# Performance work log

Measured on AMD Instinct MI355X. Metric: run time of the kernel, lower is better.

Reference implementation:

```python
import jax, jax.numpy as jnp
import numpy as np

D, FIN1, CL1_F, CL1_K, CL2_F, CL2_K, FC1_F, FC2_F = 4096, 1, 32, 25, 64, 25, 512, 10
B = 64
NNZ1, NNZ2 = D * 8, (D // 2) * 8
LMAX = 2.0  # lmax_L of a normalized graph Laplacian
FC1FIN = CL2_F * (D // 4)


def setup_inputs() -> dict:
    key = jax.random.key(0)
    ks = jax.random.split(key, 16)
    def lin(kw, fout, fin):
        scale = np.sqrt(2.0 / (fin + fout)).astype(np.float32)
        return jax.random.uniform(kw, (fout, fin), jnp.float32, -scale, scale)
    V2 = D // 2
    return {
        "x": jax.random.normal(ks[0], (B, D, FIN1), jnp.float32),
        "L1_rows": jax.random.randint(ks[1], (NNZ1,), 0, D),
        "L1_cols": jax.random.randint(ks[2], (NNZ1,), 0, D),
        "L1_vals": jax.random.normal(ks[3], (NNZ1,), jnp.float32) * 0.1,
        "L2_rows": jax.random.randint(ks[4], (NNZ2,), 0, V2),
        "L2_cols": jax.random.randint(ks[5], (NNZ2,), 0, V2),
        "L2_vals": jax.random.normal(ks[6], (NNZ2,), jnp.float32) * 0.1,
        "cl1_W": lin(ks[7], CL1_F, CL1_K * FIN1),
        "cl1_b": jnp.zeros((CL1_F,), jnp.float32),
        "cl2_W": lin(ks[8], CL2_F, CL2_K * CL1_F),
        "cl2_b": jnp.zeros((CL2_F,), jnp.float32),
        "fc1_W": lin(ks[9], FC1_F, FC1FIN),
        "fc1_b": jnp.zeros((FC1_F,), jnp.float32),
        "fc2_W": lin(ks[10], FC2_F, FC1_F),
        "fc2_b": jnp.zeros((FC2_F,), jnp.float32),
    }


def _cheby_conv(x, rows, cols, vals, W, b, K):
    # x: [B, V, Fin]; sparse rescaled Laplacian Ls = (2/lmax)*L - I applied as SpMM.
    Bn, V, Fin = x.shape
    x0 = jnp.transpose(x, (1, 2, 0)).reshape(V, Fin * Bn)  # [V, Fin*B]
    coef = jnp.asarray(2.0 / LMAX, x.dtype)

    def Ls(z):  # (2/lmax) * L @ z - z, via segment-sum SpMM
        return coef * jax.ops.segment_sum(vals[:, None] * z[cols], rows, num_segments=V) - z

    xs = [x0]
    if K > 1:
        x1 = Ls(x0)
        xs.append(x1)
    for _ in range(2, K):
        x2 = 2.0 * Ls(x1) - x0
        xs.append(x2)
        x0, x1 = x1, x2
    xk = jnp.stack(xs, 0).reshape(K, V, Fin, Bn)        # [K, V, Fin, B]
    xk = jnp.transpose(xk, (3, 1, 2, 0)).reshape(Bn * V, Fin * K)
    y = xk @ W.T + b
    return y.reshape(Bn, V, -1)


def _max_pool(x, p):
    # max-pool over node dim with stride p (matches MaxPool1d over permuted layout)
    Bn, V, F = x.shape
    return x.reshape(Bn, V // p, p, F).max(axis=2)


def reference(x, L1_rows, L1_cols, L1_vals, L2_rows, L2_cols, L2_vals,
              cl1_W, cl1_b, cl2_W, cl2_b, fc1_W, fc1_b, fc2_W, fc2_b):
    h = _cheby_conv(x, L1_rows, L1_cols, L1_vals, cl1_W, cl1_b, CL1_K)
    h = jax.nn.relu(h)
    h = _max_pool(h, 2)
    h = _cheby_conv(h, L2_rows, L2_cols, L2_vals, cl2_W, cl2_b, CL2_K)
    h = jax.nn.relu(h)
    h = _max_pool(h, 2)
    h = h.reshape(-1, FC1FIN)
    h = jax.nn.relu(h @ fc1_W.T + fc1_b)
    # dropout d=0.0 (eval/deterministic) -> identity
    return h @ fc2_W.T + fc2_b
```

## Files before the change

kernel.cpp:

```cpp
#include <hip/hip_runtime.h>
#include <hip/hip_bf16.h>

#define V1 4096
#define V2 2048
#define NNZ1 32768
#define NNZ2 16384
#define WCAP 48

typedef unsigned short u16;
typedef unsigned int u32;
typedef __attribute__((ext_vector_type(8))) short bf16x8;
typedef __attribute__((ext_vector_type(4))) float f32x4;

static __device__ __forceinline__ float bf2f(u16 u) {
  union { u32 i; float f; } c; c.i = ((u32)u) << 16; return c.f;
}
static __device__ __forceinline__ u16 f2bf(float f) {
  union { u32 i; float f; } c; c.f = f;
  u32 r = c.i + 0x7FFFu + ((c.i >> 16) & 1u);
  return (u16)(r >> 16);
}

__global__ void k_hist(const int* __restrict__ L1r, const int* __restrict__ L2r,
                       const float* __restrict__ W2, u16* __restrict__ Wh,
                       u16* __restrict__ Wl,
                       int* __restrict__ cnt1, int* __restrict__ cnt2) {
  int lt = blockIdx.x, t = threadIdx.x;
  if (lt < 128) {
    atomicAdd(&cnt1[L1r[lt * 256 + t]], 1);
  } else if (lt < 192) {
    atomicAdd(&cnt2[L2r[(lt - 128) * 256 + t]], 1);
  } else {
    int idx = (lt - 192) * 256 + t;
    int f = idx / 800;
    int kap = idx - f * 800;
    int k = kap >> 5, fin = kap & 31;
    float w = W2[f * 800 + fin * 25 + k];
    u16 hi = f2bf(w);
    Wh[idx] = hi;
    Wl[idx] = f2bf(w - bf2f(hi));
  }
}

__global__ void k_scan(int* __restrict__ cnt1, int* __restrict__ rs1,
                       int* __restrict__ cnt2, int* __restrict__ rs2,
                       int* __restrict__ slotOf1, int* __restrict__ rowOf1,
                       int* __restrict__ slotOf2, int* __restrict__ rowOf2) {
  __shared__ int sums[256];
  __shared__ int degS[V1];
  __shared__ int hist[64];
  __shared__ int hb[64];
  int t = threadIdx.x;
  int* cnt; int* rs; int* slotOf; int* rowOf; int V, NT, nnz;
  if (blockIdx.x == 0) { cnt = cnt1; rs = rs1; slotOf = slotOf1; rowOf = rowOf1; V = V1; NT = 1024; nnz = NNZ1; }
  else                 { cnt = cnt2; rs = rs2; slotOf = slotOf2; rowOf = rowOf2; V = V2; NT = 512;  nnz = NNZ2; }
  int chunk = V / 256, base = t * chunk, s = 0;
  for (int i = 0; i < chunk; ++i) { int c = cnt[base + i]; degS[base + i] = c; s += c; }
  sums[t] = s;
  if (t < 64) hist[t] = 0;
  __syncthreads();
  if (t == 0) {
    int run = 0;
    for (int i = 0; i < 256; ++i) { int c = sums[i]; sums[i] = run; run += c; }
  }
  __syncthreads();
  int pfx = sums[t];
  for (int i = 0; i < chunk; ++i) {
    int c = degS[base + i];
    rs[base + i] = pfx;
    cnt[base + i] = pfx;
    pfx += c;
  }
  if (t == 0) rs[V] = nnz;
  for (int i = 0; i < chunk; ++i) {
    int d = degS[base + i]; if (d > 63) d = 63;
    atomicAdd(&hist[d], 1);
  }
  __syncthreads();
  if (t == 0) {
    int run = 0;
    for (int d = 63; d >= 0; --d) { hb[d] = run; run += hist[d]; }
  }
  __syncthreads();
  for (int i = 0; i < chunk; ++i) {
    int v = base + i;
    int d = degS[v]; if (d > 63) d = 63;
    int r = atomicAdd(&hb[d], 1);
    int slot = (r & 3) * NT + (r >> 2);
    slotOf[v] = slot;
    rowOf[slot] = v;
  }
}

__global__ void k_scatter(const int* __restrict__ L1r, const int* __restrict__ L1c,
                          const float* __restrict__ L1v,
                          const int* __restrict__ L2r, const int* __restrict__ L2c,
                          const float* __restrict__ L2v,
                          int* __restrict__ cur1, const int* __restrict__ rs1,
                          const int* __restrict__ slotOf1, float2* __restrict__ ell1,
                          int* __restrict__ cur2, const int* __restrict__ rs2,
                          const int* __restrict__ slotOf2, float2* __restrict__ ell2) {
  int lt = blockIdx.x, t = threadIdx.x;
  if (lt < 128) {
    int e = lt * 256 + t;
    int row = L1r[e];
    int pos = atomicAdd(&cur1[row], 1);
    int w = pos - rs1[row];
    if (w < WCAP)
      ell1[(size_t)w * V1 + slotOf1[row]] = make_float2(L1v[e], __int_as_float(L1c[e] * 4));
  } else {
    int e = (lt - 128) * 256 + t;
    int row = L2r[e];
    int pos = atomicAdd(&cur2[row], 1);
    int w = pos - rs2[row];
    if (w < WCAP)
      ell2[(size_t)w * V2 + slotOf2[row]] = make_float2(L2v[e], __int_as_float(L2c[e] * 16));
  }
}

__global__ void __launch_bounds__(1024) k_l1rec(
    const float* __restrict__ x, const int* __restrict__ rs1,
    const int* __restrict__ rowOf1, const float2* __restrict__ ell1,
    u16* __restrict__ T1) {
  __shared__ float fa[V1];
  const int b = blockIdx.x, t = threadIdx.x;
#pragma unroll
  for (int j = 0; j < 4; ++j) {
    int v = t + j * 1024;
    float xv = x[(size_t)b * V1 + v];
    fa[v] = xv;
    T1[((size_t)b) * V1 + v] = f2bf(xv);
  }
  int vj[4];
#pragma unroll
  for (int j = 0; j < 4; ++j) vj[j] = rowOf1[t + j * 1024];
  int bound = rs1[vj[0] + 1] - rs1[vj[0]];
  if (bound > WCAP) bound = WCAP;
  float t2r[4];
  __syncthreads();
  for (int k = 1; k < 25; ++k) {
    float acc[4] = {0.f, 0.f, 0.f, 0.f};
    for (int w = 0; w < bound; ++w) {
      const float2* ep = ell1 + (size_t)w * V1 + t;
#pragma unroll
      for (int j = 0; j < 4; ++j) {
        float2 ev = ep[j * 1024];
        int ub = __float_as_int(ev.y);
        float av = *(const float*)((const char*)fa + ub);
        acc[j] = fmaf(ev.x, av, acc[j]);
      }
    }
    __syncthreads();
#pragma unroll
    for (int j = 0; j < 4; ++j) {
      float old = fa[vj[j]];
      float z = acc[j] - old;
      if (k > 1) z = 2.f * z - t2r[j];
      t2r[j] = old;
      fa[vj[j]] = z;
    }
    __syncthreads();
#pragma unroll
    for (int j = 0; j < 4; ++j) {
      int v = t + j * 1024;
      T1[((size_t)k * 64 + b) * V1 + v] = f2bf(fa[v]);
    }
  }
}

__global__ void k_conv1(const u16* __restrict__ T1, const float* __restrict__ W1,
                        const float* __restrict__ b1, float* __restrict__ z0) {
  __shared__ float w1s[800];
  __shared__ float b1s[32];
  const int b = blockIdx.x & 63, uc = blockIdx.x >> 6, t = threadIdx.x;
  for (int idx = t; idx < 800; idx += 256) w1s[idx] = W1[idx];
  if (t < 32) b1s[t] = b1[t];
  __syncthreads();
  const int u = uc * 256 + t;
  float a1[25], a2[25];
#pragma unroll
  for (int k = 0; k < 25; ++k) {
    u32 w = *(const u32*)&T1[((size_t)k * 64 + b) * V1 + 2 * u];
    a1[k] = bf2f((u16)w);
    a2[k] = bf2f((u16)(w >> 16));
  }
  float mout[32];
#pragma unroll
  for (int f = 0; f < 32; ++f) {
    float s1 = b1s[f], s2 = b1s[f];
#pragma unroll
    for (int k = 0; k < 25; ++k) {
      float w = w1s[f * 25 + k];
      s1 = fmaf(a1[k], w, s1);
      s2 = fmaf(a2[k], w, s2);
    }
    mout[f] = fmaxf(fmaxf(s1, 0.f), fmaxf(s2, 0.f));
  }
  float4* dst = (float4*)&z0[((size_t)b * V2 + u) * 32];
#pragma unroll
  for (int q = 0; q < 8; ++q)
    dst[q] = make_float4(mout[4 * q], mout[4 * q + 1], mout[4 * q + 2], mout[4 * q + 3]);
}

__global__ void __launch_bounds__(512, 4) k_l2rec(
    const float* __restrict__ z0, const int* __restrict__ rs2,
    const int* __restrict__ rowOf2, const float2* __restrict__ ell2,
    u16* __restrict__ T2, int b0, int bs) {
  __shared__ float TkS[V2 * 4];
  const int bl = blockIdx.x % bs, fg = blockIdx.x / bs;
  const int b = b0 + bl, f0 = fg * 4;
  const int t = threadIdx.x;
  const size_t M = (size_t)bs * V2;
  const size_t mb = (size_t)bl * V2;
#pragma unroll
  for (int j = 0; j < 4; ++j) {
    int v = t + j * 512;
    float4 xv = *(const float4*)&z0[((size_t)b * V2 + v) * 32 + f0];
    *(float4*)&TkS[v * 4] = xv;
    u32 lo = (u32)f2bf(xv.x) | ((u32)f2bf(xv.y) << 16);
    u32 hi = (u32)f2bf(xv.z) | ((u32)f2bf(xv.w) << 16);
    *(uint2*)&T2[((size_t)fg * M + mb + v) * 4] = make_uint2(lo, hi);
  }
  int vj[4];
#pragma unroll
  for (int j = 0; j < 4; ++j) vj[j] = rowOf2[t + j * 512];
  int bound = rs2[vj[0] + 1] - rs2[vj[0]];
  if (bound > WCAP) bound = WCAP;
  float4 t2r[4];
  __syncthreads();
  for (int k = 1; k < 25; ++k) {
    float4 acc[4];
#pragma unroll
    for (int j = 0; j < 4; ++j) acc[j] = make_float4(0.f, 0.f, 0.f, 0.f);
    for (int w = 0; w < bound; ++w) {
      const float2* ep = ell2 + (size_t)w * V2 + t;
#pragma unroll
      for (int j = 0; j < 4; ++j) {
        float2 ev = ep[j * 512];
        int ub = __float_as_int(ev.y);
        float4 tv = *(const float4*)((const char*)TkS + ub);
        acc[j].x = fmaf(ev.x, tv.x, acc[j].x);
        acc[j].y = fmaf(ev.x, tv.y, acc[j].y);
        acc[j].z = fmaf(ev.x, tv.z, acc[j].z);
        acc[j].w = fmaf(ev.x, tv.w, acc[j].w);
      }
    }
    __syncthreads();
#pragma unroll
    for (int j = 0; j < 4; ++j) {
      float4 old = *(const float4*)&TkS[vj[j] * 4];
      float4 z;
      z.x = acc[j].x - old.x; z.y = acc[j].y - old.y;
      z.z = acc[j].z - old.z; z.w = acc[j].w - old.w;
      if (k > 1) {
        z.x = 2.f * z.x - t2r[j].x; z.y = 2.f * z.y - t2r[j].y;
        z.z = 2.f * z.z - t2r[j].z; z.w = 2.f * z.w - t2r[j].w;
      }
      t2r[j] = old;
      *(float4*)&TkS[vj[j] * 4] = z;
    }
    __syncthreads();
#pragma unroll
    for (int j = 0; j < 4; ++j) {
      int v = t + j * 512;
      float4 zz = *(const float4*)&TkS[v * 4];
      u32 lo = (u32)f2bf(zz.x) | ((u32)f2bf(zz.y) << 16);
      u32 hi = (u32)f2bf(zz.z) | ((u32)f2bf(zz.w) << 16);
      *(uint2*)&T2[(((size_t)k * 8 + fg) * M + mb + v) * 4] = make_uint2(lo, hi);
    }
  }
}

__global__ void __launch_bounds__(256) k_conv2mm(
    const u16* __restrict__ T2, const u16* __restrict__ Wh, const u16* __restrict__ Wl,
    const float* __restrict__ b2, float* __restrict__ h2, int b0, int bs) {
  const int t = threadIdx.x;
  const int wid = t >> 6, lane = t & 63;
  const int ln = lane & 15, kg = lane >> 4;
  const size_t M = (size_t)bs * V2;
  const int mBlk = blockIdx.x * 128;
  const int bl = mBlk >> 11;
  const int v0 = mBlk & (V2 - 1);
  const int m0 = mBlk + wid * 32;
  const int vw = v0 + wid * 32;

  f32x4 acc[2][4];
#pragma unroll
  for (int nt = 0; nt < 4; ++nt) {
    float bv = b2[nt * 16 + ln];
    acc[0][nt] = (f32x4){bv, bv, bv, bv};
    acc[1][nt] = acc[0][nt];
  }

  for (int kc = 0; kc < 25; ++kc) {
    const int coff = kc * 32 + kg * 8;
    bf16x8 bh[4], blo[4];
#pragma unroll
    for (int nt = 0; nt < 4; ++nt) {
      bh[nt]  = *(const bf16x8*)(Wh + (size_t)(nt * 16 + ln) * 800 + coff);
      blo[nt] = *(const bf16x8*)(Wl + (size_t)(nt * 16 + ln) * 800 + coff);
    }
#pragma unroll
    for (int sp = 0; sp < 2; ++sp) {
      const u16* ap = T2 + ((size_t)(kc * 8 + kg * 2) * M + (size_t)(m0 + sp * 16 + ln)) * 4;
      uint2 alo = *(const uint2*)ap;
      uint2 ahi = *(const uint2*)(ap + M * 4);
      union { uint4 u; bf16x8 v; } ac;
      ac.u = make_uint4(alo.x, alo.y, ahi.x, ahi.y);
#pragma unroll
      for (int nt = 0; nt < 4; ++nt) {
        acc[sp][nt] = __builtin_amdgcn_mfma_f32_16x16x32_bf16(ac.v, bh[nt], acc[sp][nt], 0, 0, 0);
        acc[sp][nt] = __builtin_amdgcn_mfma_f32_16x16x32_bf16(ac.v, blo[nt], acc[sp][nt], 0, 0, 0);
      }
    }
  }
  const int b = b0 + bl;
  float* hrow = h2 + (size_t)b * 65536;
#pragma unroll
  for (int sp = 0; sp < 2; ++sp) {
    int u = ((vw + sp * 16) >> 1) + kg * 2;
#pragma unroll
    for (int nt = 0; nt < 4; ++nt) {
      int f = nt * 16 + ln;
      float p0 = fmaxf(fmaxf(acc[sp][nt].x, acc[sp][nt].y), 0.f);
      float p1 = fmaxf(fmaxf(acc[sp][nt].z, acc[sp][nt].w), 0.f);
      hrow[(size_t)u * 64 + f] = p0;
      hrow[(size_t)(u + 1) * 64 + f] = p1;
    }
  }
}

__global__ void __launch_bounds__(256) k_fc1(
    const float* __restrict__ h2, const float* __restrict__ fW1,
    float* __restrict__ fc1o) {
  __shared__ float wS[16 * 128];
  __shared__ float hS[64 * 129];
  const int jt = blockIdx.x & 31, ks = blockIdx.x >> 5;
  const int j0 = jt * 16, k0 = ks * 2048;
  const int t = threadIdx.x;
  const int b = t & 63, jl = t >> 6;
  float acc[4] = {0.f, 0.f, 0.f, 0.f};
  for (int kc = 0; kc < 16; ++kc) {
    int kbase = k0 + kc * 128;
    __syncthreads();
    for (int fi = t; fi < 2048; fi += 256) {
      int rowj = fi >> 7, col = fi & 127;
      wS[rowj * 128 + col] = fW1[(size_t)(j0 + rowj) * 65536 + kbase + col];
    }
    for (int fi = t; fi < 8192; fi += 256) {
      int bb = fi >> 7, kl = fi & 127;
      hS[bb * 129 + kl] = h2[(size_t)bb * 65536 + kbase + kl];
    }
    __syncthreads();
    for (int kl = 0; kl < 128; ++kl) {
      float hv = hS[b * 129 + kl];
#pragma unroll
      for (int q = 0; q < 4; ++q) acc[q] = fmaf(hv, wS[(jl * 4 + q) * 128 + kl], acc[q]);
    }
  }
#pragma unroll
  for (int q = 0; q < 4; ++q) atomicAdd(&fc1o[(j0 + jl * 4 + q) * 64 + b], acc[q]);
}

__global__ void __launch_bounds__(256) k_fc2(
    const float* __restrict__ fc1o, const float* __restrict__ fb1,
    const float* __restrict__ fW2, const float* __restrict__ fb2,
    float* __restrict__ out) {
  __shared__ float red[256];
  const int c = blockIdx.x, t = threadIdx.x;
  const int b = t & 63, g = t >> 6;
  float s = 0.f;
  for (int j = g * 128; j < g * 128 + 128; ++j) {
    float a = fmaxf(fc1o[j * 64 + b] + fb1[j], 0.f);
    s = fmaf(a, fW2[c * 512 + j], s);
  }
  red[t] = s;
  __syncthreads();
  if (t < 64) {
    out[b * 10 + c] = red[t] + red[t + 64] + red[t + 128] + red[t + 192] + fb2[c];
  }
}

extern "C" void kernel_launch(void* const* d_in, const int* in_sizes, int n_in,
                              void* d_out, int out_size, void* d_ws, size_t ws_size,
                              hipStream_t stream) {
  const float* x    = (const float*)d_in[0];
  const int* L1r    = (const int*)d_in[1];
  const int* L1c    = (const int*)d_in[2];
  const float* L1v  = (const float*)d_in[3];
  const int* L2r    = (const int*)d_in[4];
  const int* L2c    = (const int*)d_in[5];
  const float* L2v  = (const float*)d_in[6];
  const float* W1   = (const float*)d_in[7];
  const float* b1   = (const float*)d_in[8];
  const float* W2   = (const float*)d_in[9];
  const float* b2   = (const float*)d_in[10];
  const float* fW1  = (const float*)d_in[11];
  const float* fb1  = (const float*)d_in[12];
  const float* fW2  = (const float*)d_in[13];
  const float* fb2  = (const float*)d_in[14];
  float* out = (float*)d_out;

  float* Wf = (float*)d_ws;
  size_t off = 0;
  auto alloc = [&](size_t n) { float* q = Wf + off; off += n; return q; };
  int* cnt1    = (int*)alloc(4096);
  int* rs1     = (int*)alloc(4104);
  int* cnt2    = (int*)alloc(2048);
  int* rs2     = (int*)alloc(2056);
  int* slotOf1 = (int*)alloc(4096);
  int* rowOf1  = (int*)alloc(4096);
  int* slotOf2 = (int*)alloc(2048);
  int* rowOf2  = (int*)alloc(2048);
  u16* Wh      = (u16*)alloc(25600);
  u16* Wl      = (u16*)alloc(25600);
  float* fc1o  = alloc(32768);
  float2* ell1 = (float2*)alloc((size_t)WCAP * V1 * 2);
  float2* ell2 = (float2*)alloc((size_t)WCAP * V2 * 2);
  float* z0    = alloc(4194304);
  float* h2    = alloc(4194304);
  size_t fixedB = off * 4;

  int ns = 8;
  for (int c = 1; c <= 8; c <<= 1) {
    size_t t2b = (size_t)V2 * (64 / c) * 800 * 2;
    size_t big = t2b > 16777216ull ? t2b : 16777216ull;
    if (fixedB + big + 65536 <= ws_size) { ns = c; break; }
  }
  const int bs = 64 / ns;
  u16* T1 = (u16*)(Wf + off);
  u16* T2 = (u16*)(Wf + off);

  hipMemsetAsync(cnt1, 0, 4096 * sizeof(int), stream);
  hipMemsetAsync(cnt2, 0, 2048 * sizeof(int), stream);
  hipMemsetAsync(fc1o, 0, 32768 * sizeof(float), stream);
  hipMemsetAsync(ell1, 0, (size_t)WCAP * V1 * 8, stream);
  hipMemsetAsync(ell2, 0, (size_t)WCAP * V2 * 8, stream);

  k_hist<<<392, 256, 0, stream>>>(L1r, L2r, W2, Wh, Wl, cnt1, cnt2);
  k_scan<<<2, 256, 0, stream>>>(cnt1, rs1, cnt2, rs2, slotOf1, rowOf1, slotOf2, rowOf2);
  k_scatter<<<192, 256, 0, stream>>>(L1r, L1c, L1v, L2r, L2c, L2v,
                                     cnt1, rs1, slotOf1, ell1,
                                     cnt2, rs2, slotOf2, ell2);

  k_l1rec<<<64, 1024, 0, stream>>>(x, rs1, rowOf1, ell1, T1);
  k_conv1<<<512, 256, 0, stream>>>(T1, W1, b1, z0);

  for (int s = 0; s < ns; ++s) {
    int b0 = s * bs;
    k_l2rec<<<bs * 8, 512, 0, stream>>>(z0, rs2, rowOf2, ell2, T2, b0, bs);
    k_conv2mm<<<bs * 16, 256, 0, stream>>>(T2, Wh, Wl, b2, h2, b0, bs);
  }

  k_fc1<<<1024, 256, 0, stream>>>(h2, fW1, fc1o);
  k_fc2<<<10, 256, 0, stream>>>(fc1o, fb1, fW2, fb2, out);
}
```

Baseline: 846.9 us.

## Move fc1 onto bf16 MFMA with split-precision activations and weights

conv2mm now stores its pooled output as a bf16 hi/lo pair instead of fp32. The scalar-FMA fc1 kernel is replaced by an MFMA kernel that stages the hi/lo activations in swizzled shared memory. It splits the fp32 fc1 weights into hi/lo bf16 on the fly and runs three MFMAs per tile to keep close to fp32 accuracy. This targets the FMA-bound fc1 cost and cuts activation traffic. In exchange it adds per-load weight conversion work, and the dropped lo*lo term introduces a small precision loss.

```diff
diff --git a/kernel.cpp b/kernel.cpp
--- a/kernel.cpp
+++ b/kernel.cpp
@@ -273,7 +273,8 @@
 
 __global__ void __launch_bounds__(256) k_conv2mm(
     const u16* __restrict__ T2, const u16* __restrict__ Wh, const u16* __restrict__ Wl,
-    const float* __restrict__ b2, float* __restrict__ h2, int b0, int bs) {
+    const float* __restrict__ b2, u16* __restrict__ h2h, u16* __restrict__ h2l,
+    int b0, int bs) {
   const int t = threadIdx.x;
   const int wid = t >> 6, lane = t & 63;
   const int ln = lane & 15, kg = lane >> 4;
@@ -315,7 +316,8 @@
     }
   }
   const int b = b0 + bl;
-  float* hrow = h2 + (size_t)b * 65536;
+  u16* hh = h2h + (size_t)b * 65536;
+  u16* hl = h2l + (size_t)b * 65536;
 #pragma unroll
   for (int sp = 0; sp < 2; ++sp) {
     int u = ((vw + sp * 16) >> 1) + kg * 2;
@@ -324,42 +326,74 @@
       int f = nt * 16 + ln;
       float p0 = fmaxf(fmaxf(acc[sp][nt].x, acc[sp][nt].y), 0.f);
       float p1 = fmaxf(fmaxf(acc[sp][nt].z, acc[sp][nt].w), 0.f);
-      hrow[(size_t)u * 64 + f] = p0;
-      hrow[(size_t)(u + 1) * 64 + f] = p1;
-    }
-  }
-}
-
-__global__ void __launch_bounds__(256) k_fc1(
-    const float* __restrict__ h2, const float* __restrict__ fW1,
-    float* __restrict__ fc1o) {
-  __shared__ float wS[16 * 128];
-  __shared__ float hS[64 * 129];
-  const int jt = blockIdx.x & 31, ks = blockIdx.x >> 5;
-  const int j0 = jt * 16, k0 = ks * 2048;
+      u16 h0 = f2bf(p0), h1 = f2bf(p1);
+      hh[(size_t)u * 64 + f] = h0;
+      hh[(size_t)(u + 1) * 64 + f] = h1;
+      hl[(size_t)u * 64 + f] = f2bf(p0 - bf2f(h0));
+      hl[(size_t)(u + 1) * 64 + f] = f2bf(p1 - bf2f(h1));
+    }
+  }
+}
+
+__global__ void __launch_bounds__(256) k_fc1mm(
+    const u16* __restrict__ h2h, const u16* __restrict__ h2l,
+    const float* __restrict__ fW1, float* __restrict__ fc1o) {
+  __shared__ u16 ahS[64 * 128];
+  __shared__ u16 alS[64 * 128];
   const int t = threadIdx.x;
-  const int b = t & 63, jl = t >> 6;
-  float acc[4] = {0.f, 0.f, 0.f, 0.f};
-  for (int kc = 0; kc < 16; ++kc) {
-    int kbase = k0 + kc * 128;
-    __syncthreads();
-    for (int fi = t; fi < 2048; fi += 256) {
-      int rowj = fi >> 7, col = fi & 127;
-      wS[rowj * 128 + col] = fW1[(size_t)(j0 + rowj) * 65536 + kbase + col];
-    }
-    for (int fi = t; fi < 8192; fi += 256) {
-      int bb = fi >> 7, kl = fi & 127;
-      hS[bb * 129 + kl] = h2[(size_t)bb * 65536 + kbase + kl];
-    }
-    __syncthreads();
-    for (int kl = 0; kl < 128; ++kl) {
-      float hv = hS[b * 129 + kl];
-#pragma unroll
-      for (int q = 0; q < 4; ++q) acc[q] = fmaf(hv, wS[(jl * 4 + q) * 128 + kl], acc[q]);
-    }
-  }
-#pragma unroll
-  for (int q = 0; q < 4; ++q) atomicAdd(&fc1o[(j0 + jl * 4 + q) * 64 + b], acc[q]);
+  const int wid = t >> 6, lane = t & 63;
+  const int ln = lane & 15, kg = lane >> 4;
+  const int jg = blockIdx.x & 7, ksp = blockIdx.x >> 3;
+  const int j = (jg * 4 + wid) * 16 + ln;
+  const int k0 = ksp * 2048;
+
+  f32x4 acc[4];
+#pragma unroll
+  for (int bt = 0; bt < 4; ++bt) acc[bt] = (f32x4){0.f, 0.f, 0.f, 0.f};
+
+  for (int sc = 0; sc < 16; ++sc) {
+    const int kc = k0 + sc * 128;
+    __syncthreads();
+    for (int idx = t; idx < 1024; idx += 256) {
+      int row = idx >> 4, unit = idx & 15;
+      int lb = row * 256 + ((unit * 16) ^ ((row & 7) << 4));
+      *(uint4*)((char*)ahS + lb) = *(const uint4*)(h2h + (size_t)row * 65536 + kc + unit * 8);
+      *(uint4*)((char*)alS + lb) = *(const uint4*)(h2l + (size_t)row * 65536 + kc + unit * 8);
+    }
+    __syncthreads();
+#pragma unroll
+    for (int ks = 0; ks < 4; ++ks) {
+      const float* wp = fW1 + (size_t)j * 65536 + kc + ks * 32 + kg * 8;
+      float4 w0 = *(const float4*)wp;
+      float4 w1 = *(const float4*)(wp + 4);
+      float wa[8] = {w0.x, w0.y, w0.z, w0.w, w1.x, w1.y, w1.z, w1.w};
+      bf16x8 bh, bl;
+#pragma unroll
+      for (int i = 0; i < 8; ++i) {
+        u16 hi = f2bf(wa[i]);
+        ((u16*)&bh)[i] = (short)hi;
+        ((u16*)&bl)[i] = (short)f2bf(wa[i] - bf2f(hi));
+      }
+      const int kb = ks * 64 + kg * 16;
+#pragma unroll
+      for (int bt = 0; bt < 4; ++bt) {
+        int row = bt * 16 + ln;
+        int lb = row * 256 + (kb ^ ((row & 7) << 4));
+        bf16x8 ah = *(const bf16x8*)((const char*)ahS + lb);
+        bf16x8 al = *(const bf16x8*)((const char*)alS + lb);
+        acc[bt] = __builtin_amdgcn_mfma_f32_16x16x32_bf16(ah, bh, acc[bt], 0, 0, 0);
+        acc[bt] = __builtin_amdgcn_mfma_f32_16x16x32_bf16(ah, bl, acc[bt], 0, 0, 0);
+        acc[bt] = __builtin_amdgcn_mfma_f32_16x16x32_bf16(al, bh, acc[bt], 0, 0, 0);
+      }
+    }
+  }
+#pragma unroll
+  for (int bt = 0; bt < 4; ++bt) {
+#pragma unroll
+    for (int r = 0; r < 4; ++r) {
+      atomicAdd(&fc1o[(size_t)j * 64 + bt * 16 + kg * 4 + r], acc[bt][r]);
+    }
+  }
 }
 
 __global__ void __launch_bounds__(256) k_fc2(
@@ -418,7 +452,8 @@
   float2* ell1 = (float2*)alloc((size_t)WCAP * V1 * 2);
   float2* ell2 = (float2*)alloc((size_t)WCAP * V2 * 2);
   float* z0    = alloc(4194304);
-  float* h2    = alloc(4194304);
+  u16* h2h     = (u16*)alloc(2097152);
+  u16* h2l     = (u16*)alloc(2097152);
   size_t fixedB = off * 4;
 
   int ns = 8;
@@ -449,9 +484,9 @@
   for (int s = 0; s < ns; ++s) {
     int b0 = s * bs;
     k_l2rec<<<bs * 8, 512, 0, stream>>>(z0, rs2, rowOf2, ell2, T2, b0, bs);
-    k_conv2mm<<<bs * 16, 256, 0, stream>>>(T2, Wh, Wl, b2, h2, b0, bs);
-  }
-
-  k_fc1<<<1024, 256, 0, stream>>>(h2, fW1, fc1o);
+    k_conv2mm<<<bs * 16, 256, 0, stream>>>(T2, Wh, Wl, b2, h2h, h2l, b0, bs);
+  }
+
+  k_fc1mm<<<256, 256, 0, stream>>>(h2h, h2l, fW1, fc1o);
   k_fc2<<<10, 256, 0, stream>>>(fc1o, fb1, fW2, fb2, out);
 }
```

New measurement: 729.9 us. 1.16x faster.
